# Kernel tuning notes

Measured on AMD Instinct MI355X. Metric: run time of the kernel, lower is better.

## Reference

```python
import jax, jax.numpy as jnp
import numpy as np

N = 16384
E = 524288
F_IN, F_HID, F_OUT = 128, 256, 128
EPS = 1e-5


def setup_inputs() -> dict:
    key = jax.random.key(0)
    ks = jax.random.split(key, 8)
    x = jax.random.normal(ks[0], (N, F_IN), dtype=jnp.float32)
    edge_index = jax.random.randint(ks[1], (2, E), 0, N, dtype=jnp.int64)
    edge_weight = jax.random.uniform(ks[2], (E,), dtype=jnp.float32)
    # Linear params stored as [in, out] (y = x @ W + b; same math as torch Linear)
    W1_w = jax.random.normal(ks[3], (F_IN, F_HID), dtype=jnp.float32) / np.sqrt(F_IN)
    W1_b = jnp.zeros((F_HID,), dtype=jnp.float32)
    W2_w = jax.random.normal(ks[4], (F_HID, F_OUT), dtype=jnp.float32) / np.sqrt(F_HID)
    W2_b = jnp.zeros((F_OUT,), dtype=jnp.float32)
    ln_g = jnp.ones((F_HID,), dtype=jnp.float32)
    ln_b = jnp.zeros((F_HID,), dtype=jnp.float32)
    return {"x": x, "edge_index": edge_index, "edge_weight": edge_weight,
            "W1_w": W1_w, "W1_b": W1_b, "W2_w": W2_w, "W2_b": W2_b,
            "ln_g": ln_g, "ln_b": ln_b}


def _layernorm(h, g, b):
    mu = jnp.mean(h, axis=-1, keepdims=True)
    var = jnp.var(h, axis=-1, keepdims=True)
    return (h - mu) * jax.lax.rsqrt(var + EPS) * g + b


def reference(x, edge_index, edge_weight, W1_w, W1_b, W2_w, W2_b, ln_g, ln_b):
    n = x.shape[0]
    adj = jnp.zeros((n, n), dtype=x.dtype).at[edge_index[0], edge_index[1]].set(edge_weight)
    adj = adj + jnp.eye(n, dtype=x.dtype)
    degree = jnp.clip(adj.sum(axis=1, keepdims=True), 1.0, None)
    adj = adj / degree
    h = jnp.matmul(adj, x) @ W1_w + W1_b          # [N, F_HID]
    h = jax.nn.relu(_layernorm(h, ln_g, ln_b))
    # dropout is identity in eval mode
    out = jnp.matmul(adj, h) @ W2_w + W2_b        # [N, F_OUT]
    return out
```

## Files before the change

kernel.cpp:

```cpp
#include <hip/hip_runtime.h>

#define N_NODES 16384
#define F_IN    128
#define F_HID   256
#define F_OUT   128
#define LN_EPS  1e-5f
#define CAP     128
#define HSTR    264

typedef __attribute__((ext_vector_type(8))) short bf16x8;
typedef __attribute__((ext_vector_type(4))) float f32x4;

__device__ __forceinline__ unsigned short bf16rne(float f) {
    unsigned u = __float_as_uint(f);
    unsigned r = (u + 0x7fffu + ((u >> 16) & 1u)) >> 16;
    return (unsigned short)r;
}
__device__ __forceinline__ float bf_lo(unsigned v) { return __uint_as_float(v << 16); }
__device__ __forceinline__ float bf_hi(unsigned v) { return __uint_as_float(v & 0xffff0000u); }

__global__ void prelude_kernel(const float* __restrict__ x, unsigned short* __restrict__ xb,
                               const float* __restrict__ W1, unsigned short* __restrict__ W1t,
                               const float* __restrict__ W2, unsigned short* __restrict__ W2t,
                               int* __restrict__ cur, const unsigned* __restrict__ ei,
                               int* __restrict__ mode) {
    int b = blockIdx.x, t = threadIdx.x;
    if (b < 2048) {
        int i = (b * 256 + t) * 4;
        float4 v = *(const float4*)&x[i];
        ushort4 o;
        o.x = bf16rne(v.x); o.y = bf16rne(v.y); o.z = bf16rne(v.z); o.w = bf16rne(v.w);
        *(ushort4*)&xb[i] = o;
    } else if (b < 2176) {
        int id = (b - 2048) * 256 + t;
        int n = id >> 7, k = id & 127;
        W1t[id] = bf16rne(W1[(size_t)k * F_HID + n]);
    } else if (b < 2304) {
        int id = (b - 2176) * 256 + t;
        int n = id >> 8, k = id & 255;
        W2t[id] = bf16rne(W2[(size_t)k * F_OUT + n]);
    } else if (b < 2368) {
        cur[(b - 2304) * 256 + t] = 0;
    } else {
        __shared__ int nz;
        if (t == 0) nz = 0;
        __syncthreads();
        for (int it = 0; it < 4; ++it) {
            int idx = 2 * (t + it * 256) + 1;
            if (ei[idx] != 0u) nz = 1;
        }
        __syncthreads();
        if (t == 0) *mode = (nz == 0) ? 1 : 0;
    }
}

__global__ void fill_kernel(const void* __restrict__ ei, const int* __restrict__ mode,
                            int* __restrict__ cur, int2* __restrict__ ed, int E) {
    int base = blockIdx.x * 1024 + threadIdx.x;
    int m = *mode;
#pragma unroll
    for (int u = 0; u < 4; ++u) {
        int e = base + u * 256;
        if (e >= E) continue;
        int r, c;
        if (m) {
            const long long* p = (const long long*)ei;
            r = (int)p[e]; c = (int)p[e + E];
        } else {
            const int* p = (const int*)ei;
            r = p[e]; c = p[e + E];
        }
        if (((unsigned)r | (unsigned)c) >= N_NODES) continue;
        int pos = atomicAdd(&cur[r], 1);
        if (pos < CAP) ed[r * CAP + pos] = make_int2(c, e);
    }
}

__global__ void dd_spmm1_kernel(const float* __restrict__ ew, int* __restrict__ cur,
                                int2* __restrict__ ed, float* __restrict__ invdeg,
                                const unsigned* __restrict__ xb,
                                unsigned* __restrict__ h0b) {
    __shared__ int   scol[4][CAP];
    __shared__ int   seid[4][CAP];
    __shared__ float sw[4][CAP];
    int wave = threadIdx.x >> 6, lane = threadIdx.x & 63;
    int r = blockIdx.x * 4 + wave;
    int d = cur[r];
    if (d > CAP) d = CAP;
    int2* row = ed + r * CAP;

    for (int i = lane; i < d; i += 64) {
        int2 e = row[i];
        scol[wave][i] = e.x;
        seid[wave][i] = e.y;
    }
    __syncthreads();

    float wsum = 0.0f;
    for (int i = lane; i < d; i += 64) {
        int myc = scol[wave][i], mye = seid[wave][i];
        bool kill = false;
        for (int j = 0; j < d; ++j)
            if (scol[wave][j] == myc && seid[wave][j] > mye) { kill = true; break; }
        float w = kill ? 0.0f : ew[mye];
        sw[wave][i] = w;
        ((int*)&row[i])[1] = __float_as_int(w);
        wsum += w;
    }
    for (int off = 32; off; off >>= 1) wsum += __shfl_xor(wsum, off, 64);
    float inv = 1.0f / (1.0f + wsum);
    if (lane == 0) { invdeg[r] = inv; cur[r] = d; }
    __syncthreads();

    unsigned self = xb[r * 64 + lane];
    float ax = bf_lo(self), ay = bf_hi(self);
    int j = 0;
    for (; j + 16 <= d; j += 16) {
        int c[16]; float w[16]; unsigned v[16];
#pragma unroll
        for (int u = 0; u < 16; ++u) { c[u] = scol[wave][j + u]; w[u] = sw[wave][j + u]; }
#pragma unroll
        for (int u = 0; u < 16; ++u) v[u] = xb[c[u] * 64 + lane];
#pragma unroll
        for (int u = 0; u < 16; ++u) { ax += w[u] * bf_lo(v[u]); ay += w[u] * bf_hi(v[u]); }
    }
    for (; j < d; ++j) {
        int cc = scol[wave][j];
        float w = sw[wave][j];
        unsigned v = xb[cc * 64 + lane];
        ax += w * bf_lo(v); ay += w * bf_hi(v);
    }
    float ox = ax * inv, oy = ay * inv;
    h0b[r * 64 + lane] = ((unsigned)bf16rne(oy) << 16) | (unsigned)bf16rne(ox);
}

__global__ void spmm2_kernel(const unsigned* __restrict__ xb, const int* __restrict__ cur,
                             const int2* __restrict__ ed, const float* __restrict__ invdeg,
                             const float* __restrict__ bias, float* __restrict__ outp) {
    int wave = threadIdx.x >> 6, lane = threadIdx.x & 63;
    int r = blockIdx.x * 4 + wave;
    const int4* rowq = (const int4*)(ed + r * CAP);
    int d = cur[r];
    if (d > CAP) d = CAP;
    unsigned self = xb[r * 64 + lane];
    float ax = bf_lo(self), ay = bf_hi(self);
    int j = 0;
    for (; j + 16 <= d; j += 16) {
        int4 q[8]; int c[16]; float w[16]; unsigned v[16];
#pragma unroll
        for (int u = 0; u < 8; ++u) q[u] = rowq[(j >> 1) + u];
#pragma unroll
        for (int u = 0; u < 8; ++u) {
            c[2 * u] = q[u].x;     w[2 * u] = __int_as_float(q[u].y);
            c[2 * u + 1] = q[u].z; w[2 * u + 1] = __int_as_float(q[u].w);
        }
#pragma unroll
        for (int u = 0; u < 16; ++u) v[u] = xb[c[u] * 64 + lane];
#pragma unroll
        for (int u = 0; u < 16; ++u) { ax += w[u] * bf_lo(v[u]); ay += w[u] * bf_hi(v[u]); }
    }
    for (; j + 4 <= d; j += 4) {
        int4 q0 = rowq[j >> 1], q1 = rowq[(j >> 1) + 1];
        unsigned v0 = xb[q0.x * 64 + lane];
        unsigned v1 = xb[q0.z * 64 + lane];
        unsigned v2 = xb[q1.x * 64 + lane];
        unsigned v3 = xb[q1.z * 64 + lane];
        float w0 = __int_as_float(q0.y), w1 = __int_as_float(q0.w);
        float w2 = __int_as_float(q1.y), w3 = __int_as_float(q1.w);
        ax += w0 * bf_lo(v0) + w1 * bf_lo(v1) + w2 * bf_lo(v2) + w3 * bf_lo(v3);
        ay += w0 * bf_hi(v0) + w1 * bf_hi(v1) + w2 * bf_hi(v2) + w3 * bf_hi(v3);
    }
    const int2* row = (const int2*)(ed + r * CAP);
    for (; j < d; ++j) {
        int2 e = row[j];
        float w = __int_as_float(e.y);
        unsigned v = xb[e.x * 64 + lane];
        ax += w * bf_lo(v); ay += w * bf_hi(v);
    }
    float inv = invdeg[r];
    float ox = ax * inv + bias[2 * lane];
    float oy = ay * inv + bias[2 * lane + 1];
    ((float2*)outp)[r * 64 + lane] = make_float2(ox, oy);
}

__launch_bounds__(256)
__global__ void mlp_mfma_kernel(const unsigned short* __restrict__ h0b,
                                const unsigned short* __restrict__ W1t,
                                const unsigned short* __restrict__ W2t,
                                const float* __restrict__ b1,
                                const float* __restrict__ ln_g, const float* __restrict__ ln_b,
                                unsigned short* __restrict__ h2b) {
    __shared__ unsigned short Hs[4][16 * HSTR];
    int t = threadIdx.x;
    int wid = t >> 6, lane = t & 63;
    int lnid = lane & 15, quad = lane >> 4;
    int R = blockIdx.x * 64 + wid * 16;
    unsigned short* H = Hs[wid];

    bf16x8 a[4];
#pragma unroll
    for (int ch = 0; ch < 4; ++ch)
        a[ch] = *(const bf16x8*)&h0b[(size_t)(R + lnid) * F_IN + ch * 32 + quad * 8];
    f32x4 acc[16];
#pragma unroll
    for (int ct = 0; ct < 16; ++ct) {
        f32x4 c = {0.0f, 0.0f, 0.0f, 0.0f};
        const unsigned short* wrow = &W1t[(size_t)(ct * 16 + lnid) * F_IN];
#pragma unroll
        for (int ch = 0; ch < 4; ++ch) {
            bf16x8 b = *(const bf16x8*)&wrow[ch * 32 + quad * 8];
            c = __builtin_amdgcn_mfma_f32_16x16x32_bf16(a[ch], b, c, 0, 0, 0);
        }
        acc[ct] = c;
    }
    float s[4] = {0, 0, 0, 0}, q[4] = {0, 0, 0, 0};
#pragma unroll
    for (int ct = 0; ct < 16; ++ct) {
        float bv = b1[ct * 16 + lnid];
#pragma unroll
        for (int r = 0; r < 4; ++r) {
            float v = acc[ct][r] + bv;
            acc[ct][r] = v;
            s[r] += v; q[r] += v * v;
        }
    }
#pragma unroll
    for (int r = 0; r < 4; ++r)
        for (int off = 1; off < 16; off <<= 1) {
            s[r] += __shfl_xor(s[r], off, 64);
            q[r] += __shfl_xor(q[r], off, 64);
        }
    float mean[4], rinv[4];
#pragma unroll
    for (int r = 0; r < 4; ++r) {
        mean[r] = s[r] * (1.0f / F_HID);
        float var = q[r] * (1.0f / F_HID) - mean[r] * mean[r];
        rinv[r] = rsqrtf(var + LN_EPS);
    }
#pragma unroll
    for (int ct = 0; ct < 16; ++ct) {
        int c = ct * 16 + lnid;
        float g = ln_g[c], bb = ln_b[c];
#pragma unroll
        for (int r = 0; r < 4; ++r) {
            float v = fmaxf((acc[ct][r] - mean[r]) * rinv[r] * g + bb, 0.0f);
            H[(quad * 4 + r) * HSTR + c] = bf16rne(v);
        }
    }
    __syncthreads();

    bf16x8 a2[8];
#pragma unroll
    for (int ch = 0; ch < 8; ++ch)
        a2[ch] = *(const bf16x8*)&H[lnid * HSTR + ch * 32 + quad * 8];
#pragma unroll
    for (int ct = 0; ct < 8; ++ct) {
        f32x4 c = {0.0f, 0.0f, 0.0f, 0.0f};
        const unsigned short* wrow = &W2t[(size_t)(ct * 16 + lnid) * F_HID];
#pragma unroll
        for (int ch = 0; ch < 8; ++ch) {
            bf16x8 b = *(const bf16x8*)&wrow[ch * 32 + quad * 8];
            c = __builtin_amdgcn_mfma_f32_16x16x32_bf16(a2[ch], b, c, 0, 0, 0);
        }
#pragma unroll
        for (int r = 0; r < 4; ++r)
            H[(quad * 4 + r) * 132 + ct * 16 + lnid] = bf16rne(c[r]);
    }
    __syncthreads();

#pragma unroll
    for (int p = 0; p < 8; ++p) {
        int flat = p * 64 + lane;
        int m = flat >> 5, cg = flat & 31;
        *(ushort4*)&h2b[(size_t)(R + m) * F_OUT + cg * 4] =
            *(const ushort4*)&H[m * 132 + cg * 4];
    }
}

extern "C" void kernel_launch(void* const* d_in, const int* in_sizes, int n_in,
                              void* d_out, int out_size, void* d_ws, size_t ws_size,
                              hipStream_t stream) {
    const float* x   = (const float*)d_in[0];
    const void*  ei  = d_in[1];
    const float* ew  = (const float*)d_in[2];
    const float* W1  = (const float*)d_in[3];
    const float* b1  = (const float*)d_in[4];
    const float* W2  = (const float*)d_in[5];
    const float* b2  = (const float*)d_in[6];
    const float* lng = (const float*)d_in[7];
    const float* lnb = (const float*)d_in[8];
    float* out = (float*)d_out;
    int E = in_sizes[2];

    char* w = (char*)d_ws;
    size_t off = 0;
    auto take = [&](size_t bytes) -> char* {
        char* p = w + off;
        off += (bytes + 255) & ~(size_t)255;
        return p;
    };
    int*   cur    = (int*)take((size_t)N_NODES * 4);
    float* invdeg = (float*)take((size_t)N_NODES * 4);
    int2*  ed     = (int2*)take((size_t)N_NODES * CAP * 8);
    unsigned short* xb  = (unsigned short*)take((size_t)N_NODES * F_IN * 2);
    unsigned short* h0b = (unsigned short*)take((size_t)N_NODES * F_IN * 2);
    unsigned short* h2b = (unsigned short*)take((size_t)N_NODES * F_OUT * 2);
    unsigned short* W1t = (unsigned short*)take((size_t)F_IN * F_HID * 2);
    unsigned short* W2t = (unsigned short*)take((size_t)F_HID * F_OUT * 2);
    int*   mode   = (int*)take(4);

    prelude_kernel<<<2369, 256, 0, stream>>>(x, xb, W1, W1t, W2, W2t, cur,
                                             (const unsigned*)ei, mode);
    fill_kernel<<<(E + 1023) / 1024, 256, 0, stream>>>(ei, mode, cur, ed, E);
    dd_spmm1_kernel<<<N_NODES / 4, 256, 0, stream>>>(ew, cur, ed, invdeg,
                                                     (const unsigned*)xb, (unsigned*)h0b);
    mlp_mfma_kernel<<<N_NODES / 64, 256, 0, stream>>>(h0b, W1t, W2t, b1, lng, lnb, h2b);
    spmm2_kernel<<<N_NODES / 4, 256, 0, stream>>>((const unsigned*)h2b, cur, ed, invdeg,
                                                  b2, out);
}
```

Before: 191.1 us.

## Fuse first-layer aggregation with MFMA MLP into one kernel via shared memory

Merges the dedup/aggregation kernel and the MLP kernel into a single kernel. Each block handles 16 rows: every wave aggregates 4 rows into shared memory, then the four waves split the W1 and W2 MFMA column tiles, with a cross-wave LayerNorm reduction done through shared memory. This removes the h0b global round trip and one launch. In exchange, each wave now processes its 4 rows one after another with block-wide barriers, and every block re-reads the weights, so per-block latency and weight traffic go up.

```diff
diff --git a/kernel.cpp b/kernel.cpp
--- a/kernel.cpp
+++ b/kernel.cpp
@@ -6,7 +6,9 @@
 #define F_OUT   128
 #define LN_EPS  1e-5f
 #define CAP     128
-#define HSTR    264
+#define H0STR   136
+#define H1STR   264
+#define REPSTR  132
 
 typedef __attribute__((ext_vector_type(8))) short bf16x8;
 typedef __attribute__((ext_vector_type(4))) float f32x4;
@@ -76,62 +78,173 @@
     }
 }
 
-__global__ void dd_spmm1_kernel(const float* __restrict__ ew, int* __restrict__ cur,
-                                int2* __restrict__ ed, float* __restrict__ invdeg,
-                                const unsigned* __restrict__ xb,
-                                unsigned* __restrict__ h0b) {
+__launch_bounds__(256)
+__global__ void agg_mlp_kernel(const float* __restrict__ ew, int* __restrict__ cur,
+                               int2* __restrict__ ed, float* __restrict__ invdeg,
+                               const unsigned* __restrict__ xb,
+                               const unsigned short* __restrict__ W1t,
+                               const unsigned short* __restrict__ W2t,
+                               const float* __restrict__ b1,
+                               const float* __restrict__ ln_g, const float* __restrict__ ln_b,
+                               unsigned short* __restrict__ h2b) {
     __shared__ int   scol[4][CAP];
     __shared__ int   seid[4][CAP];
     __shared__ float sw[4][CAP];
-    int wave = threadIdx.x >> 6, lane = threadIdx.x & 63;
-    int r = blockIdx.x * 4 + wave;
-    int d = cur[r];
-    if (d > CAP) d = CAP;
-    int2* row = ed + r * CAP;
-
-    for (int i = lane; i < d; i += 64) {
-        int2 e = row[i];
-        scol[wave][i] = e.x;
-        seid[wave][i] = e.y;
+    __shared__ unsigned short H0[16 * H0STR];
+    __shared__ unsigned short H1[16 * H1STR];
+    __shared__ float red[2][4][16];
+
+    int t = threadIdx.x, wave = t >> 6, lane = t & 63;
+    int lnid = lane & 15, quad = lane >> 4;
+    int Rbase = blockIdx.x * 16;
+
+    for (int rr = 0; rr < 4; ++rr) {
+        int r = Rbase + wave * 4 + rr;
+        int d = cur[r];
+        if (d > CAP) d = CAP;
+        int2* row = ed + (size_t)r * CAP;
+        for (int i = lane; i < d; i += 64) {
+            int2 e = row[i];
+            scol[wave][i] = e.x;
+            seid[wave][i] = e.y;
+        }
+        __syncthreads();
+
+        float wsum = 0.0f;
+        for (int i = lane; i < d; i += 64) {
+            int myc = scol[wave][i], mye = seid[wave][i];
+            bool kill = false;
+            for (int j = 0; j < d; ++j) {
+                if (scol[wave][j] == myc) {
+                    if (seid[wave][j] > mye) { kill = true; break; }
+                }
+            }
+            float w = kill ? 0.0f : ew[mye];
+            sw[wave][i] = w;
+            ((int*)&row[i])[1] = __float_as_int(w);
+            wsum += w;
+        }
+        for (int off = 32; off; off >>= 1) wsum += __shfl_xor(wsum, off, 64);
+        float inv = 1.0f / (1.0f + wsum);
+        if (lane == 0) { invdeg[r] = inv; cur[r] = d; }
+        __syncthreads();
+
+        unsigned self = xb[r * 64 + lane];
+        float ax = bf_lo(self), ay = bf_hi(self);
+        int j = 0;
+        for (; j + 16 <= d; j += 16) {
+            int c[16]; float w[16]; unsigned v[16];
+#pragma unroll
+            for (int u = 0; u < 16; ++u) { c[u] = scol[wave][j + u]; w[u] = sw[wave][j + u]; }
+#pragma unroll
+            for (int u = 0; u < 16; ++u) v[u] = xb[c[u] * 64 + lane];
+#pragma unroll
+            for (int u = 0; u < 16; ++u) { ax += w[u] * bf_lo(v[u]); ay += w[u] * bf_hi(v[u]); }
+        }
+        for (; j < d; ++j) {
+            int cc = scol[wave][j];
+            float w = sw[wave][j];
+            unsigned v = xb[cc * 64 + lane];
+            ax += w * bf_lo(v); ay += w * bf_hi(v);
+        }
+        float ox = ax * inv, oy = ay * inv;
+        unsigned pack = ((unsigned)bf16rne(oy) << 16) | (unsigned)bf16rne(ox);
+        *(unsigned*)&H0[(wave * 4 + rr) * H0STR + lane * 2] = pack;
     }
     __syncthreads();
 
-    float wsum = 0.0f;
-    for (int i = lane; i < d; i += 64) {
-        int myc = scol[wave][i], mye = seid[wave][i];
-        bool kill = false;
-        for (int j = 0; j < d; ++j)
-            if (scol[wave][j] == myc && seid[wave][j] > mye) { kill = true; break; }
-        float w = kill ? 0.0f : ew[mye];
-        sw[wave][i] = w;
-        ((int*)&row[i])[1] = __float_as_int(w);
-        wsum += w;
-    }
-    for (int off = 32; off; off >>= 1) wsum += __shfl_xor(wsum, off, 64);
-    float inv = 1.0f / (1.0f + wsum);
-    if (lane == 0) { invdeg[r] = inv; cur[r] = d; }
+    bf16x8 a[4];
+#pragma unroll
+    for (int ch = 0; ch < 4; ++ch)
+        a[ch] = *(const bf16x8*)&H0[lnid * H0STR + ch * 32 + quad * 8];
+    f32x4 acc[4];
+#pragma unroll
+    for (int p = 0; p < 4; ++p) {
+        int ct = wave * 4 + p;
+        f32x4 c = {0.0f, 0.0f, 0.0f, 0.0f};
+        const unsigned short* wrow = &W1t[(size_t)(ct * 16 + lnid) * F_IN];
+#pragma unroll
+        for (int ch = 0; ch < 4; ++ch) {
+            bf16x8 b = *(const bf16x8*)&wrow[ch * 32 + quad * 8];
+            c = __builtin_amdgcn_mfma_f32_16x16x32_bf16(a[ch], b, c, 0, 0, 0);
+        }
+        acc[p] = c;
+    }
+    float s[4] = {0, 0, 0, 0}, q[4] = {0, 0, 0, 0};
+#pragma unroll
+    for (int p = 0; p < 4; ++p) {
+        float bv = b1[(wave * 4 + p) * 16 + lnid];
+#pragma unroll
+        for (int r = 0; r < 4; ++r) {
+            float v = acc[p][r] + bv;
+            acc[p][r] = v;
+            s[r] += v; q[r] += v * v;
+        }
+    }
+#pragma unroll
+    for (int r = 0; r < 4; ++r)
+        for (int off = 1; off < 16; off <<= 1) {
+            s[r] += __shfl_xor(s[r], off, 64);
+            q[r] += __shfl_xor(q[r], off, 64);
+        }
+    if (lnid == 0) {
+#pragma unroll
+        for (int r = 0; r < 4; ++r) {
+            red[0][wave][quad * 4 + r] = s[r];
+            red[1][wave][quad * 4 + r] = q[r];
+        }
+    }
     __syncthreads();
-
-    unsigned self = xb[r * 64 + lane];
-    float ax = bf_lo(self), ay = bf_hi(self);
-    int j = 0;
-    for (; j + 16 <= d; j += 16) {
-        int c[16]; float w[16]; unsigned v[16];
-#pragma unroll
-        for (int u = 0; u < 16; ++u) { c[u] = scol[wave][j + u]; w[u] = sw[wave][j + u]; }
-#pragma unroll
-        for (int u = 0; u < 16; ++u) v[u] = xb[c[u] * 64 + lane];
-#pragma unroll
-        for (int u = 0; u < 16; ++u) { ax += w[u] * bf_lo(v[u]); ay += w[u] * bf_hi(v[u]); }
-    }
-    for (; j < d; ++j) {
-        int cc = scol[wave][j];
-        float w = sw[wave][j];
-        unsigned v = xb[cc * 64 + lane];
-        ax += w * bf_lo(v); ay += w * bf_hi(v);
-    }
-    float ox = ax * inv, oy = ay * inv;
-    h0b[r * 64 + lane] = ((unsigned)bf16rne(oy) << 16) | (unsigned)bf16rne(ox);
+    float mean[4], rinv[4];
+#pragma unroll
+    for (int r = 0; r < 4; ++r) {
+        int rowi = quad * 4 + r;
+        float S = red[0][0][rowi] + red[0][1][rowi] + red[0][2][rowi] + red[0][3][rowi];
+        float Q = red[1][0][rowi] + red[1][1][rowi] + red[1][2][rowi] + red[1][3][rowi];
+        mean[r] = S * (1.0f / F_HID);
+        float var = Q * (1.0f / F_HID) - mean[r] * mean[r];
+        rinv[r] = rsqrtf(var + LN_EPS);
+    }
+#pragma unroll
+    for (int p = 0; p < 4; ++p) {
+        int c = (wave * 4 + p) * 16 + lnid;
+        float g = ln_g[c], bb = ln_b[c];
+#pragma unroll
+        for (int r = 0; r < 4; ++r) {
+            float v = fmaxf((acc[p][r] - mean[r]) * rinv[r] * g + bb, 0.0f);
+            H1[(quad * 4 + r) * H1STR + c] = bf16rne(v);
+        }
+    }
+    __syncthreads();
+
+    bf16x8 a2[8];
+#pragma unroll
+    for (int ch = 0; ch < 8; ++ch)
+        a2[ch] = *(const bf16x8*)&H1[lnid * H1STR + ch * 32 + quad * 8];
+    unsigned short* rep = H0;
+#pragma unroll
+    for (int p = 0; p < 2; ++p) {
+        int ct = wave * 2 + p;
+        f32x4 c = {0.0f, 0.0f, 0.0f, 0.0f};
+        const unsigned short* wrow = &W2t[(size_t)(ct * 16 + lnid) * F_HID];
+#pragma unroll
+        for (int ch = 0; ch < 8; ++ch) {
+            bf16x8 b = *(const bf16x8*)&wrow[ch * 32 + quad * 8];
+            c = __builtin_amdgcn_mfma_f32_16x16x32_bf16(a2[ch], b, c, 0, 0, 0);
+        }
+#pragma unroll
+        for (int r = 0; r < 4; ++r)
+            rep[(quad * 4 + r) * REPSTR + ct * 16 + lnid] = bf16rne(c[r]);
+    }
+    __syncthreads();
+
+#pragma unroll
+    for (int p = 0; p < 2; ++p) {
+        int flat = p * 256 + t;
+        int m = flat >> 5, cg = flat & 31;
+        *(ushort4*)&h2b[(size_t)(Rbase + m) * F_OUT + cg * 4] =
+            *(const ushort4*)&rep[m * REPSTR + cg * 4];
+    }
 }
 
 __global__ void spmm2_kernel(const unsigned* __restrict__ xb, const int* __restrict__ cur,
@@ -181,100 +294,6 @@
     float ox = ax * inv + bias[2 * lane];
     float oy = ay * inv + bias[2 * lane + 1];
     ((float2*)outp)[r * 64 + lane] = make_float2(ox, oy);
-}
-
-__launch_bounds__(256)
-__global__ void mlp_mfma_kernel(const unsigned short* __restrict__ h0b,
-                                const unsigned short* __restrict__ W1t,
-                                const unsigned short* __restrict__ W2t,
-                                const float* __restrict__ b1,
-                                const float* __restrict__ ln_g, const float* __restrict__ ln_b,
-                                unsigned short* __restrict__ h2b) {
-    __shared__ unsigned short Hs[4][16 * HSTR];
-    int t = threadIdx.x;
-    int wid = t >> 6, lane = t & 63;
-    int lnid = lane & 15, quad = lane >> 4;
-    int R = blockIdx.x * 64 + wid * 16;
-    unsigned short* H = Hs[wid];
-
-    bf16x8 a[4];
-#pragma unroll
-    for (int ch = 0; ch < 4; ++ch)
-        a[ch] = *(const bf16x8*)&h0b[(size_t)(R + lnid) * F_IN + ch * 32 + quad * 8];
-    f32x4 acc[16];
-#pragma unroll
-    for (int ct = 0; ct < 16; ++ct) {
-        f32x4 c = {0.0f, 0.0f, 0.0f, 0.0f};
-        const unsigned short* wrow = &W1t[(size_t)(ct * 16 + lnid) * F_IN];
-#pragma unroll
-        for (int ch = 0; ch < 4; ++ch) {
-            bf16x8 b = *(const bf16x8*)&wrow[ch * 32 + quad * 8];
-            c = __builtin_amdgcn_mfma_f32_16x16x32_bf16(a[ch], b, c, 0, 0, 0);
-        }
-        acc[ct] = c;
-    }
-    float s[4] = {0, 0, 0, 0}, q[4] = {0, 0, 0, 0};
-#pragma unroll
-    for (int ct = 0; ct < 16; ++ct) {
-        float bv = b1[ct * 16 + lnid];
-#pragma unroll
-        for (int r = 0; r < 4; ++r) {
-            float v = acc[ct][r] + bv;
-            acc[ct][r] = v;
-            s[r] += v; q[r] += v * v;
-        }
-    }
-#pragma unroll
-    for (int r = 0; r < 4; ++r)
-        for (int off = 1; off < 16; off <<= 1) {
-            s[r] += __shfl_xor(s[r], off, 64);
-            q[r] += __shfl_xor(q[r], off, 64);
-        }
-    float mean[4], rinv[4];
-#pragma unroll
-    for (int r = 0; r < 4; ++r) {
-        mean[r] = s[r] * (1.0f / F_HID);
-        float var = q[r] * (1.0f / F_HID) - mean[r] * mean[r];
-        rinv[r] = rsqrtf(var + LN_EPS);
-    }
-#pragma unroll
-    for (int ct = 0; ct < 16; ++ct) {
-        int c = ct * 16 + lnid;
-        float g = ln_g[c], bb = ln_b[c];
-#pragma unroll
-        for (int r = 0; r < 4; ++r) {
-            float v = fmaxf((acc[ct][r] - mean[r]) * rinv[r] * g + bb, 0.0f);
-            H[(quad * 4 + r) * HSTR + c] = bf16rne(v);
-        }
-    }
-    __syncthreads();
-
-    bf16x8 a2[8];
-#pragma unroll
-    for (int ch = 0; ch < 8; ++ch)
-        a2[ch] = *(const bf16x8*)&H[lnid * HSTR + ch * 32 + quad * 8];
-#pragma unroll
-    for (int ct = 0; ct < 8; ++ct) {
-        f32x4 c = {0.0f, 0.0f, 0.0f, 0.0f};
-        const unsigned short* wrow = &W2t[(size_t)(ct * 16 + lnid) * F_HID];
-#pragma unroll
-        for (int ch = 0; ch < 8; ++ch) {
-            bf16x8 b = *(const bf16x8*)&wrow[ch * 32 + quad * 8];
-            c = __builtin_amdgcn_mfma_f32_16x16x32_bf16(a2[ch], b, c, 0, 0, 0);
-        }
-#pragma unroll
-        for (int r = 0; r < 4; ++r)
-            H[(quad * 4 + r) * 132 + ct * 16 + lnid] = bf16rne(c[r]);
-    }
-    __syncthreads();
-
-#pragma unroll
-    for (int p = 0; p < 8; ++p) {
-        int flat = p * 64 + lane;
-        int m = flat >> 5, cg = flat & 31;
-        *(ushort4*)&h2b[(size_t)(R + m) * F_OUT + cg * 4] =
-            *(const ushort4*)&H[m * 132 + cg * 4];
-    }
 }
 
 extern "C" void kernel_launch(void* const* d_in, const int* in_sizes, int n_in,
@@ -303,7 +322,6 @@
     float* invdeg = (float*)take((size_t)N_NODES * 4);
     int2*  ed     = (int2*)take((size_t)N_NODES * CAP * 8);
     unsigned short* xb  = (unsigned short*)take((size_t)N_NODES * F_IN * 2);
-    unsigned short* h0b = (unsigned short*)take((size_t)N_NODES * F_IN * 2);
     unsigned short* h2b = (unsigned short*)take((size_t)N_NODES * F_OUT * 2);
     unsigned short* W1t = (unsigned short*)take((size_t)F_IN * F_HID * 2);
     unsigned short* W2t = (unsigned short*)take((size_t)F_HID * F_OUT * 2);
@@ -312,9 +330,9 @@
     prelude_kernel<<<2369, 256, 0, stream>>>(x, xb, W1, W1t, W2, W2t, cur,
                                              (const unsigned*)ei, mode);
     fill_kernel<<<(E + 1023) / 1024, 256, 0, stream>>>(ei, mode, cur, ed, E);
-    dd_spmm1_kernel<<<N_NODES / 4, 256, 0, stream>>>(ew, cur, ed, invdeg,
-                                                     (const unsigned*)xb, (unsigned*)h0b);
-    mlp_mfma_kernel<<<N_NODES / 64, 256, 0, stream>>>(h0b, W1t, W2t, b1, lng, lnb, h2b);
+    agg_mlp_kernel<<<N_NODES / 16, 256, 0, stream>>>(ew, cur, ed, invdeg,
+                                                     (const unsigned*)xb, W1t, W2t,
+                                                     b1, lng, lnb, h2b);
     spmm2_kernel<<<N_NODES / 4, 256, 0, stream>>>((const unsigned*)h2b, cur, ed, invdeg,
                                                   b2, out);
 }
```

Result: no change. 187.8 us (-1.7%).
